# Optimization experiments

Measured on AMD Instinct MI355X. Metric: run time of the kernel, lower is better.

Reference implementation:

```python
import jax, jax.numpy as jnp
import numpy as np

NUM_USERS = 1_000_000
NUM_ITEMS = 500_000
NUM_GENRES = 20
NUM_TAGS = 100
EMBEDDING_DIM = 64
HIDDEN_UNITS = [256, 128, 64]
NUM_CLASSES = 5
BATCH = 16384


def setup_inputs() -> dict:
    key = jax.random.key(0)
    ks = jax.random.split(key, 16)
    deep_in = EMBEDDING_DIM * 2 + NUM_GENRES + NUM_TAGS  # 248
    inp = {
        "user": jax.random.randint(ks[0], (BATCH,), 0, NUM_USERS),
        "item": jax.random.randint(ks[1], (BATCH,), 0, NUM_ITEMS),
        "genre": jax.random.uniform(ks[2], (BATCH, NUM_GENRES), dtype=jnp.float32),
        "tag": jax.random.uniform(ks[3], (BATCH, NUM_TAGS), dtype=jnp.float32),
        # wide Linear(num_users+num_items -> HIDDEN_UNITS[-1]); stored transposed
        # as (vocab, out) so the one-hot matmul becomes a row gather.
        "wide_W": jax.random.normal(ks[4], (NUM_USERS + NUM_ITEMS, HIDDEN_UNITS[-1]), dtype=jnp.float32) * 0.01,
        "wide_b": jnp.zeros((HIDDEN_UNITS[-1],), dtype=jnp.float32),
        "user_emb": jax.random.normal(ks[5], (NUM_USERS, EMBEDDING_DIM), dtype=jnp.float32) * 0.01,
        "item_emb": jax.random.normal(ks[6], (NUM_ITEMS, EMBEDDING_DIM), dtype=jnp.float32) * 0.01,
        "W0": jax.random.normal(ks[7], (deep_in, HIDDEN_UNITS[0]), dtype=jnp.float32) * 0.02,
        "b0": jnp.zeros((HIDDEN_UNITS[0],), dtype=jnp.float32),
        "W1": jax.random.normal(ks[8], (HIDDEN_UNITS[0], HIDDEN_UNITS[1]), dtype=jnp.float32) * 0.02,
        "b1": jnp.zeros((HIDDEN_UNITS[1],), dtype=jnp.float32),
        "W2": jax.random.normal(ks[9], (HIDDEN_UNITS[1], HIDDEN_UNITS[2]), dtype=jnp.float32) * 0.02,
        "b2": jnp.zeros((HIDDEN_UNITS[2],), dtype=jnp.float32),
        "final_W": jax.random.normal(ks[10], (HIDDEN_UNITS[-1] * 2, NUM_CLASSES), dtype=jnp.float32) * 0.02,
        "final_b": jnp.zeros((NUM_CLASSES,), dtype=jnp.float32),
    }
    return inp


def reference(user, item, genre, tag, wide_W, wide_b, user_emb, item_emb,
              W0, b0, W1, b1, W2, b2, final_W, final_b):
    # Wide path: one_hot(user)++one_hot(item) @ W + b  ==  gather+sum of rows.
    wide_out = wide_W[user] + wide_W[NUM_USERS + item] + wide_b  # [B, 64]
    # Deep path (dropout is identity in eval mode).
    u = user_emb[user]   # [B, E]
    v = item_emb[item]   # [B, E]
    h = jnp.concatenate([u, v, genre, tag], axis=1)  # [B, 248]
    h = jax.nn.relu(h @ W0 + b0)
    h = jax.nn.relu(h @ W1 + b1)
    h = jax.nn.relu(h @ W2 + b2)  # [B, 64]
    combined = jnp.concatenate([h, wide_out], axis=1)  # [B, 128]
    logits = combined @ final_W + final_b  # [B, NUM_CLASSES]
    return logits
```

## Files before the change

### kernel.cpp

```cpp
#include <hip/hip_runtime.h>

#define BATCH 16384
#define NU 1000000
#define TBR 32
#define MT 512
#define WSOFF0 0
#define WSOFF1 65536
#define WSOFF2 98304
#define WSREQ  212992

typedef __attribute__((ext_vector_type(8))) short short8;
typedef __attribute__((ext_vector_type(4))) short short4v;
typedef __attribute__((ext_vector_type(4))) float f32x4;

__device__ __forceinline__ unsigned short f32_bf16(float f) {
    unsigned int u = __float_as_uint(f);
    u += 0x7FFF + ((u >> 16) & 1);
    return (unsigned short)(u >> 16);
}
__device__ __forceinline__ float bf16_f32(unsigned short h) {
    return __uint_as_float(((unsigned int)h) << 16);
}

__device__ __forceinline__ int swz(int row, int byteInRow, int rowStrideB) {
    return row * rowStrideB + (byteInRow ^ ((row & 7) << 4));
}

__device__ __forceinline__ short8 cvt8(float4 a, float4 b) {
    short8 s;
    s[0] = (short)f32_bf16(a.x); s[1] = (short)f32_bf16(a.y);
    s[2] = (short)f32_bf16(a.z); s[3] = (short)f32_bf16(a.w);
    s[4] = (short)f32_bf16(b.x); s[5] = (short)f32_bf16(b.y);
    s[6] = (short)f32_bf16(b.z); s[7] = (short)f32_bf16(b.w);
    return s;
}

__global__ void prep_weights(const float* __restrict__ W0, const float* __restrict__ W1,
                             const float* __restrict__ W2, unsigned short* __restrict__ ws)
{
    __shared__ float t[64 * 65];
    int b = blockIdx.x;
    const float* src; unsigned short* dst; int K, N, K2, k0, n0;
    if (b < 16)      { src = W0; dst = ws + WSOFF0; K = 248; N = 256; K2 = 256; k0 = (b >> 2) * 64; n0 = (b & 3) * 64; }
    else if (b < 24) { int i = b - 16; src = W1; dst = ws + WSOFF1; K = 256; N = 128; K2 = 256; k0 = (i >> 1) * 64; n0 = (i & 1) * 64; }
    else             { int i = b - 24; src = W2; dst = ws + WSOFF2; K = 128; N = 64;  K2 = 128; k0 = i * 64; n0 = 0; }

    int tid = threadIdx.x;
    for (int q = tid; q < 64 * 16; q += 256) {
        int k = q >> 4, nq = q & 15;
        float4 v = make_float4(0.f, 0.f, 0.f, 0.f);
        if (k0 + k < K) v = *(const float4*)(src + (size_t)(k0 + k) * N + n0 + nq * 4);
        t[k * 65 + nq * 4 + 0] = v.x;
        t[k * 65 + nq * 4 + 1] = v.y;
        t[k * 65 + nq * 4 + 2] = v.z;
        t[k * 65 + nq * 4 + 3] = v.w;
    }
    __syncthreads();
    for (int q = tid; q < 64 * 8; q += 256) {
        int n = q >> 3, kg = q & 7;
        short8 o;
        #pragma unroll
        for (int i = 0; i < 8; ++i) o[i] = (short)f32_bf16(t[(kg * 8 + i) * 65 + n]);
        *(short8*)(dst + (size_t)(n0 + n) * K2 + k0 + kg * 8) = o;
    }
}

__global__ __launch_bounds__(MT) void wd_mfma(
        const int* __restrict__ user, const int* __restrict__ item,
        const float* __restrict__ genre, const float* __restrict__ tag,
        const float* __restrict__ wide_W, const float* __restrict__ wide_b,
        const float* __restrict__ user_emb, const float* __restrict__ item_emb,
        const float* __restrict__ b0, const float* __restrict__ b1,
        const float* __restrict__ b2,
        const float* __restrict__ fW, const float* __restrict__ fb,
        const unsigned short* __restrict__ ws, float* __restrict__ out)
{
    __shared__ unsigned short sX[TBR * 256];
    __shared__ unsigned short sH0[TBR * 256];
    __shared__ unsigned short sH1[TBR * 128];
    __shared__ unsigned short sH2[TBR * 72];
    __shared__ unsigned short sWide[TBR * 72];

    const int tid = threadIdx.x;
    const int row0 = blockIdx.x * TBR;
    const unsigned short* w0t = ws + WSOFF0;
    const unsigned short* w1t = ws + WSOFF1;
    const unsigned short* w2t = ws + WSOFF2;

    for (int q = tid; q < TBR * 32; q += MT) {
        int r = q >> 5, j = q & 31;
        int grow = row0 + r;
        float4 va = make_float4(0.f, 0.f, 0.f, 0.f);
        float4 vb = va;
        if (j < 8) {
            const float4* p = (const float4*)(user_emb + (size_t)user[grow] * 64);
            va = p[j * 2]; vb = p[j * 2 + 1];
        } else if (j < 16) {
            const float4* p = (const float4*)(item_emb + (size_t)item[grow] * 64);
            va = p[(j - 8) * 2]; vb = p[(j - 8) * 2 + 1];
        } else if (j == 16) {
            const float4* p = (const float4*)(genre + (size_t)grow * 20);
            va = p[0]; vb = p[1];
        } else if (j == 17) {
            const float4* p = (const float4*)(genre + (size_t)grow * 20);
            va = p[2]; vb = p[3];
        } else if (j == 18) {
            va = *(const float4*)(genre + (size_t)grow * 20 + 16);
            vb = *(const float4*)(tag + (size_t)grow * 100);
        } else if (j < 31) {
            const float4* p = (const float4*)(tag + (size_t)grow * 100 + 4);
            int jj = j - 19;
            va = p[jj * 2]; vb = p[jj * 2 + 1];
        }
        *(short8*)((char*)sX + swz(r, j * 16, 512)) = cvt8(va, vb);
    }

    for (int q = tid; q < TBR * 16; q += MT) {
        int r = q >> 4, j = q & 15;
        int grow = row0 + r;
        float4 a = ((const float4*)(wide_W + (size_t)user[grow] * 64))[j];
        float4 b = ((const float4*)(wide_W + (size_t)(NU + item[grow]) * 64))[j];
        float4 c = ((const float4*)wide_b)[j];
        short4v o;
        o[0] = (short)f32_bf16(a.x + b.x + c.x);
        o[1] = (short)f32_bf16(a.y + b.y + c.y);
        o[2] = (short)f32_bf16(a.z + b.z + c.z);
        o[3] = (short)f32_bf16(a.w + b.w + c.w);
        *(short4v*)(sWide + r * 72 + j * 4) = o;
    }
    __syncthreads();

    const int wid = tid >> 6;
    const int lane = tid & 63;
    const int lr = lane & 15;
    const int lh = lane >> 4;

    {
        const int cbase = wid * 32;
        f32x4 acc[2][2];
        #pragma unroll
        for (int rt = 0; rt < 2; ++rt)
            #pragma unroll
            for (int t = 0; t < 2; ++t) acc[rt][t] = (f32x4)(0.f);

        #pragma unroll
        for (int kc = 0; kc < 8; ++kc) {
            const int kb = kc * 32 + lh * 8;
            short8 a[2];
            #pragma unroll
            for (int rt = 0; rt < 2; ++rt)
                a[rt] = *(const short8*)((const char*)sX + swz(rt * 16 + lr, kb * 2, 512));
            #pragma unroll
            for (int t = 0; t < 2; ++t) {
                short8 bf = *(const short8*)(w0t + (size_t)(cbase + t * 16 + lr) * 256 + kb);
                #pragma unroll
                for (int rt = 0; rt < 2; ++rt)
                    acc[rt][t] = __builtin_amdgcn_mfma_f32_16x16x32_bf16(a[rt], bf, acc[rt][t], 0, 0, 0);
            }
        }
        #pragma unroll
        for (int t = 0; t < 2; ++t) {
            float bias = b0[cbase + t * 16 + lr];
            #pragma unroll
            for (int rt = 0; rt < 2; ++rt)
                #pragma unroll
                for (int jj = 0; jj < 4; ++jj) {
                    int row = rt * 16 + lh * 4 + jj;
                    float v = fmaxf(acc[rt][t][jj] + bias, 0.f);
                    *(unsigned short*)((char*)sH0 + swz(row, (cbase + t * 16 + lr) * 2, 512)) = f32_bf16(v);
                }
        }
        __syncthreads();
    }

    {
        const int cbase = wid * 16;
        f32x4 acc[2];
        acc[0] = (f32x4)(0.f); acc[1] = (f32x4)(0.f);

        #pragma unroll
        for (int kc = 0; kc < 8; ++kc) {
            const int kb = kc * 32 + lh * 8;
            short8 a[2];
            #pragma unroll
            for (int rt = 0; rt < 2; ++rt)
                a[rt] = *(const short8*)((const char*)sH0 + swz(rt * 16 + lr, kb * 2, 512));
            short8 bf = *(const short8*)(w1t + (size_t)(cbase + lr) * 256 + kb);
            #pragma unroll
            for (int rt = 0; rt < 2; ++rt)
                acc[rt] = __builtin_amdgcn_mfma_f32_16x16x32_bf16(a[rt], bf, acc[rt], 0, 0, 0);
        }
        float bias = b1[cbase + lr];
        #pragma unroll
        for (int rt = 0; rt < 2; ++rt)
            #pragma unroll
            for (int jj = 0; jj < 4; ++jj) {
                int row = rt * 16 + lh * 4 + jj;
                float v = fmaxf(acc[rt][jj] + bias, 0.f);
                *(unsigned short*)((char*)sH1 + swz(row, (cbase + lr) * 2, 256)) = f32_bf16(v);
            }
        __syncthreads();
    }

    {
        const int t = wid & 3;
        const int rtb = wid >> 2;
        const int cbase = t * 16;
        f32x4 acc = (f32x4)(0.f);

        #pragma unroll
        for (int kc = 0; kc < 4; ++kc) {
            const int kb = kc * 32 + lh * 8;
            short8 a = *(const short8*)((const char*)sH1 + swz(rtb * 16 + lr, kb * 2, 256));
            short8 bf = *(const short8*)(w2t + (size_t)(cbase + lr) * 128 + kb);
            acc = __builtin_amdgcn_mfma_f32_16x16x32_bf16(a, bf, acc, 0, 0, 0);
        }
        float bias = b2[cbase + lr];
        #pragma unroll
        for (int jj = 0; jj < 4; ++jj) {
            int row = rtb * 16 + lh * 4 + jj;
            sH2[row * 72 + cbase + lr] = f32_bf16(fmaxf(acc[jj] + bias, 0.f));
        }
        __syncthreads();
    }

    if (tid < TBR * 5) {
        int r = tid / 5, c = tid - r * 5;
        float acc = fb[c];
        #pragma unroll
        for (int kq = 0; kq < 8; ++kq) {
            short8 h = *(const short8*)(sH2 + r * 72 + kq * 8);
            #pragma unroll
            for (int i = 0; i < 8; ++i)
                acc = fmaf(bf16_f32((unsigned short)h[i]), fW[(kq * 8 + i) * 5 + c], acc);
        }
        #pragma unroll
        for (int kq = 0; kq < 8; ++kq) {
            short8 h = *(const short8*)(sWide + r * 72 + kq * 8);
            #pragma unroll
            for (int i = 0; i < 8; ++i)
                acc = fmaf(bf16_f32((unsigned short)h[i]), fW[(64 + kq * 8 + i) * 5 + c], acc);
        }
        out[(size_t)(row0 + r) * 5 + c] = acc;
    }
}

#define NTHR 256
#define TB 32

__device__ __forceinline__ void fma4(float4& a, float s, const float4& w) {
    a.x = fmaf(s, w.x, a.x); a.y = fmaf(s, w.y, a.y);
    a.z = fmaf(s, w.z, a.z); a.w = fmaf(s, w.w, a.w);
}
__device__ __forceinline__ float4 add4(const float4& a, const float4& b) {
    return make_float4(a.x + b.x, a.y + b.y, a.z + b.z, a.w + b.w);
}
__device__ __forceinline__ float4 relu4(const float4& a) {
    return make_float4(fmaxf(a.x, 0.f), fmaxf(a.y, 0.f), fmaxf(a.z, 0.f), fmaxf(a.w, 0.f));
}

__global__ void wd_fused(const int* __restrict__ user, const int* __restrict__ item,
                         const float* __restrict__ genre, const float* __restrict__ tag,
                         const float* __restrict__ wide_W, const float* __restrict__ wide_b,
                         const float* __restrict__ user_emb, const float* __restrict__ item_emb,
                         const float* __restrict__ W0, const float* __restrict__ b0,
                         const float* __restrict__ W1, const float* __restrict__ b1,
                         const float* __restrict__ W2, const float* __restrict__ b2,
                         const float* __restrict__ fW, const float* __restrict__ fb,
                         float* __restrict__ out)
{
    __shared__ float sA[TB * 248];
    __shared__ float sB[TB * 256];
    __shared__ float sC[TB * 64];

    const int tid = threadIdx.x;
    const int row0 = blockIdx.x * TB;

    for (int q = tid; q < TB * 62; q += NTHR) {
        int r = q / 62, j = q - r * 62, grow = row0 + r;
        float4 v;
        if (j < 16) v = reinterpret_cast<const float4*>(user_emb + (size_t)user[grow] * 64)[j];
        else if (j < 32) v = reinterpret_cast<const float4*>(item_emb + (size_t)item[grow] * 64)[j - 16];
        else if (j < 37) v = reinterpret_cast<const float4*>(genre + (size_t)grow * 20)[j - 32];
        else v = reinterpret_cast<const float4*>(tag + (size_t)grow * 100)[j - 37];
        *reinterpret_cast<float4*>(sA + r * 248 + j * 4) = v;
    }
    for (int q = tid; q < TB * 16; q += NTHR) {
        int r = q >> 4, j = q & 15, grow = row0 + r;
        float4 a = reinterpret_cast<const float4*>(wide_W + (size_t)user[grow] * 64)[j];
        float4 b = reinterpret_cast<const float4*>(wide_W + (size_t)(NU + item[grow]) * 64)[j];
        float4 c = reinterpret_cast<const float4*>(wide_b)[j];
        *reinterpret_cast<float4*>(sC + r * 64 + j * 4) =
            make_float4(a.x + b.x + c.x, a.y + b.y + c.y, a.z + b.z + c.z, a.w + b.w + c.w);
    }
    __syncthreads();
    {
        const int cg = tid & 63, r0 = (tid >> 6) * 8;
        float4 acc[8];
        #pragma unroll
        for (int r = 0; r < 8; ++r) acc[r] = make_float4(0.f, 0.f, 0.f, 0.f);
        for (int k = 0; k < 248; k += 4) {
            const float4* wp = reinterpret_cast<const float4*>(W0 + (size_t)k * 256) + cg;
            float4 w0 = wp[0], w1 = wp[64], w2 = wp[128], w3 = wp[192];
            #pragma unroll
            for (int r = 0; r < 8; ++r) {
                float4 xv = *reinterpret_cast<const float4*>(sA + (r0 + r) * 248 + k);
                fma4(acc[r], xv.x, w0); fma4(acc[r], xv.y, w1);
                fma4(acc[r], xv.z, w2); fma4(acc[r], xv.w, w3);
            }
        }
        float4 bb = reinterpret_cast<const float4*>(b0)[cg];
        #pragma unroll
        for (int r = 0; r < 8; ++r)
            *reinterpret_cast<float4*>(sB + (r0 + r) * 256 + cg * 4) = relu4(add4(acc[r], bb));
    }
    __syncthreads();
    {
        const int cg = tid & 31, r0 = (tid >> 5) * 4;
        float4 acc[4];
        #pragma unroll
        for (int r = 0; r < 4; ++r) acc[r] = make_float4(0.f, 0.f, 0.f, 0.f);
        for (int k = 0; k < 256; k += 4) {
            const float4* wp = reinterpret_cast<const float4*>(W1 + (size_t)k * 128) + cg;
            float4 w0 = wp[0], w1 = wp[32], w2 = wp[64], w3 = wp[96];
            #pragma unroll
            for (int r = 0; r < 4; ++r) {
                float4 xv = *reinterpret_cast<const float4*>(sB + (r0 + r) * 256 + k);
                fma4(acc[r], xv.x, w0); fma4(acc[r], xv.y, w1);
                fma4(acc[r], xv.z, w2); fma4(acc[r], xv.w, w3);
            }
        }
        float4 bb = reinterpret_cast<const float4*>(b1)[cg];
        #pragma unroll
        for (int r = 0; r < 4; ++r)
            *reinterpret_cast<float4*>(sA + (r0 + r) * 128 + cg * 4) = relu4(add4(acc[r], bb));
    }
    __syncthreads();
    {
        const int cg = tid & 15, r0 = (tid >> 4) * 2;
        float4 acc[2];
        acc[0] = make_float4(0.f, 0.f, 0.f, 0.f); acc[1] = acc[0];
        for (int k = 0; k < 128; k += 4) {
            const float4* wp = reinterpret_cast<const float4*>(W2 + (size_t)k * 64) + cg;
            float4 w0 = wp[0], w1 = wp[16], w2 = wp[32], w3 = wp[48];
            #pragma unroll
            for (int r = 0; r < 2; ++r) {
                float4 xv = *reinterpret_cast<const float4*>(sA + (r0 + r) * 128 + k);
                fma4(acc[r], xv.x, w0); fma4(acc[r], xv.y, w1);
                fma4(acc[r], xv.z, w2); fma4(acc[r], xv.w, w3);
            }
        }
        float4 bb = reinterpret_cast<const float4*>(b2)[cg];
        #pragma unroll
        for (int r = 0; r < 2; ++r)
            *reinterpret_cast<float4*>(sB + (r0 + r) * 64 + cg * 4) = relu4(add4(acc[r], bb));
    }
    __syncthreads();
    if (tid < TB * 5) {
        int r = tid / 5, c = tid - r * 5;
        float acc = fb[c];
        for (int k = 0; k < 64; ++k) acc = fmaf(sB[r * 64 + k], fW[k * 5 + c], acc);
        for (int k = 0; k < 64; ++k) acc = fmaf(sC[r * 64 + k], fW[(64 + k) * 5 + c], acc);
        out[(size_t)(row0 + r) * 5 + c] = acc;
    }
}

extern "C" void kernel_launch(void* const* d_in, const int* in_sizes, int n_in,
                              void* d_out, int out_size, void* d_ws, size_t ws_size,
                              hipStream_t stream) {
    const int* user = (const int*)d_in[0];
    const int* item = (const int*)d_in[1];
    const float* genre = (const float*)d_in[2];
    const float* tag = (const float*)d_in[3];
    const float* wide_W = (const float*)d_in[4];
    const float* wide_b = (const float*)d_in[5];
    const float* user_emb = (const float*)d_in[6];
    const float* item_emb = (const float*)d_in[7];
    const float* W0 = (const float*)d_in[8];
    const float* b0 = (const float*)d_in[9];
    const float* W1 = (const float*)d_in[10];
    const float* b1 = (const float*)d_in[11];
    const float* W2 = (const float*)d_in[12];
    const float* b2 = (const float*)d_in[13];
    const float* fW = (const float*)d_in[14];
    const float* fb = (const float*)d_in[15];
    float* out = (float*)d_out;

    if (ws_size >= (size_t)WSREQ) {
        hipLaunchKernelGGL(prep_weights, dim3(26), dim3(256), 0, stream,
                           W0, W1, W2, (unsigned short*)d_ws);
        hipLaunchKernelGGL(wd_mfma, dim3(BATCH / TBR), dim3(MT), 0, stream,
                           user, item, genre, tag, wide_W, wide_b, user_emb, item_emb,
                           b0, b1, b2, fW, fb, (const unsigned short*)d_ws, out);
    } else {
        hipLaunchKernelGGL(wd_fused, dim3(BATCH / TB), dim3(NTHR), 0, stream,
                           user, item, genre, tag, wide_W, wide_b, user_emb, item_emb,
                           W0, b0, W1, b1, W2, b2, fW, fb, out);
    }
}
```

Measured before the change: 34.36 us.

## Double rows per block, preload layer weights into registers, stage final weights in LDS

Rows per block go from 32 to 64. Each wave now loads its W0 and W1 bf16 fragments and the biases into registers once, before the gather phase, so those global weight loads overlap the embedding gathers. Each fragment is then reused across four row tiles instead of two. The gather loops are fully unrolled into a fixed six iterations, and the final 640-float weight matrix is staged in shared memory. The kernel launches half as many blocks, and launch_bounds(512,1) plus the larger register weight arrays raise register use and lower occupancy. That may reduce latency hiding for the random gathers.

```diff
diff --git a/kernel.cpp b/kernel.cpp
--- a/kernel.cpp
+++ b/kernel.cpp
@@ -2,7 +2,7 @@
 
 #define BATCH 16384
 #define NU 1000000
-#define TBR 32
+#define TBR 64
 #define MT 512
 #define WSOFF0 0
 #define WSOFF1 65536
@@ -65,7 +65,7 @@
     }
 }
 
-__global__ __launch_bounds__(MT) void wd_mfma(
+__global__ __launch_bounds__(MT, 1) void wd_mfma(
         const int* __restrict__ user, const int* __restrict__ item,
         const float* __restrict__ genre, const float* __restrict__ tag,
         const float* __restrict__ wide_W, const float* __restrict__ wide_b,
@@ -80,6 +80,7 @@
     __shared__ unsigned short sH1[TBR * 128];
     __shared__ unsigned short sH2[TBR * 72];
     __shared__ unsigned short sWide[TBR * 72];
+    __shared__ float sFW[640];
 
     const int tid = threadIdx.x;
     const int row0 = blockIdx.x * TBR;
@@ -87,140 +88,162 @@
     const unsigned short* w1t = ws + WSOFF1;
     const unsigned short* w2t = ws + WSOFF2;
 
-    for (int q = tid; q < TBR * 32; q += MT) {
-        int r = q >> 5, j = q & 31;
-        int grow = row0 + r;
-        float4 va = make_float4(0.f, 0.f, 0.f, 0.f);
-        float4 vb = va;
-        if (j < 8) {
-            const float4* p = (const float4*)(user_emb + (size_t)user[grow] * 64);
-            va = p[j * 2]; vb = p[j * 2 + 1];
-        } else if (j < 16) {
-            const float4* p = (const float4*)(item_emb + (size_t)item[grow] * 64);
-            va = p[(j - 8) * 2]; vb = p[(j - 8) * 2 + 1];
-        } else if (j == 16) {
-            const float4* p = (const float4*)(genre + (size_t)grow * 20);
-            va = p[0]; vb = p[1];
-        } else if (j == 17) {
-            const float4* p = (const float4*)(genre + (size_t)grow * 20);
-            va = p[2]; vb = p[3];
-        } else if (j == 18) {
-            va = *(const float4*)(genre + (size_t)grow * 20 + 16);
-            vb = *(const float4*)(tag + (size_t)grow * 100);
-        } else if (j < 31) {
-            const float4* p = (const float4*)(tag + (size_t)grow * 100 + 4);
-            int jj = j - 19;
-            va = p[jj * 2]; vb = p[jj * 2 + 1];
-        }
-        *(short8*)((char*)sX + swz(r, j * 16, 512)) = cvt8(va, vb);
-    }
-
-    for (int q = tid; q < TBR * 16; q += MT) {
-        int r = q >> 4, j = q & 15;
-        int grow = row0 + r;
-        float4 a = ((const float4*)(wide_W + (size_t)user[grow] * 64))[j];
-        float4 b = ((const float4*)(wide_W + (size_t)(NU + item[grow]) * 64))[j];
-        float4 c = ((const float4*)wide_b)[j];
-        short4v o;
-        o[0] = (short)f32_bf16(a.x + b.x + c.x);
-        o[1] = (short)f32_bf16(a.y + b.y + c.y);
-        o[2] = (short)f32_bf16(a.z + b.z + c.z);
-        o[3] = (short)f32_bf16(a.w + b.w + c.w);
-        *(short4v*)(sWide + r * 72 + j * 4) = o;
-    }
-    __syncthreads();
-
     const int wid = tid >> 6;
     const int lane = tid & 63;
     const int lr = lane & 15;
     const int lh = lane >> 4;
 
-    {
-        const int cbase = wid * 32;
-        f32x4 acc[2][2];
-        #pragma unroll
-        for (int rt = 0; rt < 2; ++rt)
+    const int cb0 = wid * 32;
+    const int cb1 = wid * 16;
+    short8 B0[2][8];
+    #pragma unroll
+    for (int t = 0; t < 2; ++t)
+        #pragma unroll
+        for (int kc = 0; kc < 8; ++kc)
+            B0[t][kc] = *(const short8*)(w0t + (size_t)(cb0 + t * 16 + lr) * 256 + kc * 32 + lh * 8);
+    short8 B1[8];
+    #pragma unroll
+    for (int kc = 0; kc < 8; ++kc)
+        B1[kc] = *(const short8*)(w1t + (size_t)(cb1 + lr) * 256 + kc * 32 + lh * 8);
+    float rb0[2];
+    rb0[0] = b0[cb0 + lr]; rb0[1] = b0[cb0 + 16 + lr];
+    float rb1 = b1[cb1 + lr];
+    float rb2 = b2[(wid & 3) * 16 + lr];
+
+    #pragma unroll
+    for (int it = 0; it < 6; ++it) {
+        int q = tid + it * MT;
+        if (it < 4) {
+            int r = q >> 5, j = q & 31;
+            int grow = row0 + r;
+            float4 va = make_float4(0.f, 0.f, 0.f, 0.f);
+            float4 vb = va;
+            if (j < 8) {
+                const float4* p = (const float4*)(user_emb + (size_t)user[grow] * 64);
+                va = p[j * 2]; vb = p[j * 2 + 1];
+            } else if (j < 16) {
+                const float4* p = (const float4*)(item_emb + (size_t)item[grow] * 64);
+                va = p[(j - 8) * 2]; vb = p[(j - 8) * 2 + 1];
+            } else if (j == 16) {
+                const float4* p = (const float4*)(genre + (size_t)grow * 20);
+                va = p[0]; vb = p[1];
+            } else if (j == 17) {
+                const float4* p = (const float4*)(genre + (size_t)grow * 20);
+                va = p[2]; vb = p[3];
+            } else if (j == 18) {
+                va = *(const float4*)(genre + (size_t)grow * 20 + 16);
+                vb = *(const float4*)(tag + (size_t)grow * 100);
+            } else if (j < 31) {
+                const float4* p = (const float4*)(tag + (size_t)grow * 100 + 4);
+                int jj = j - 19;
+                va = p[jj * 2]; vb = p[jj * 2 + 1];
+            }
+            *(short8*)((char*)sX + swz(r, j * 16, 512)) = cvt8(va, vb);
+        } else {
+            int p = q - 4 * MT;
+            int r = p >> 4, j = p & 15;
+            int grow = row0 + r;
+            float4 a = ((const float4*)(wide_W + (size_t)user[grow] * 64))[j];
+            float4 b = ((const float4*)(wide_W + (size_t)(NU + item[grow]) * 64))[j];
+            float4 c = ((const float4*)wide_b)[j];
+            short4v o;
+            o[0] = (short)f32_bf16(a.x + b.x + c.x);
+            o[1] = (short)f32_bf16(a.y + b.y + c.y);
+            o[2] = (short)f32_bf16(a.z + b.z + c.z);
+            o[3] = (short)f32_bf16(a.w + b.w + c.w);
+            *(short4v*)(sWide + r * 72 + j * 4) = o;
+        }
+    }
+    if (tid < 160) {
+        ((float4*)sFW)[tid] = ((const float4*)fW)[tid];
+    }
+    __syncthreads();
+
+    {
+        f32x4 acc[4][2];
+        #pragma unroll
+        for (int rt = 0; rt < 4; ++rt)
             #pragma unroll
             for (int t = 0; t < 2; ++t) acc[rt][t] = (f32x4)(0.f);
 
         #pragma unroll
         for (int kc = 0; kc < 8; ++kc) {
             const int kb = kc * 32 + lh * 8;
-            short8 a[2];
-            #pragma unroll
-            for (int rt = 0; rt < 2; ++rt)
+            short8 a[4];
+            #pragma unroll
+            for (int rt = 0; rt < 4; ++rt)
                 a[rt] = *(const short8*)((const char*)sX + swz(rt * 16 + lr, kb * 2, 512));
             #pragma unroll
-            for (int t = 0; t < 2; ++t) {
-                short8 bf = *(const short8*)(w0t + (size_t)(cbase + t * 16 + lr) * 256 + kb);
+            for (int t = 0; t < 2; ++t)
                 #pragma unroll
-                for (int rt = 0; rt < 2; ++rt)
-                    acc[rt][t] = __builtin_amdgcn_mfma_f32_16x16x32_bf16(a[rt], bf, acc[rt][t], 0, 0, 0);
-            }
+                for (int rt = 0; rt < 4; ++rt)
+                    acc[rt][t] = __builtin_amdgcn_mfma_f32_16x16x32_bf16(a[rt], B0[t][kc], acc[rt][t], 0, 0, 0);
         }
         #pragma unroll
         for (int t = 0; t < 2; ++t) {
-            float bias = b0[cbase + t * 16 + lr];
-            #pragma unroll
-            for (int rt = 0; rt < 2; ++rt)
+            #pragma unroll
+            for (int rt = 0; rt < 4; ++rt)
                 #pragma unroll
                 for (int jj = 0; jj < 4; ++jj) {
                     int row = rt * 16 + lh * 4 + jj;
-                    float v = fmaxf(acc[rt][t][jj] + bias, 0.f);
-                    *(unsigned short*)((char*)sH0 + swz(row, (cbase + t * 16 + lr) * 2, 512)) = f32_bf16(v);
+                    float v = fmaxf(acc[rt][t][jj] + rb0[t], 0.f);
+                    *(unsigned short*)((char*)sH0 + swz(row, (cb0 + t * 16 + lr) * 2, 512)) = f32_bf16(v);
                 }
         }
         __syncthreads();
     }
 
     {
-        const int cbase = wid * 16;
+        f32x4 acc[4];
+        #pragma unroll
+        for (int rt = 0; rt < 4; ++rt) acc[rt] = (f32x4)(0.f);
+
+        #pragma unroll
+        for (int kc = 0; kc < 8; ++kc) {
+            const int kb = kc * 32 + lh * 8;
+            short8 a[4];
+            #pragma unroll
+            for (int rt = 0; rt < 4; ++rt)
+                a[rt] = *(const short8*)((const char*)sH0 + swz(rt * 16 + lr, kb * 2, 512));
+            #pragma unroll
+            for (int rt = 0; rt < 4; ++rt)
+                acc[rt] = __builtin_amdgcn_mfma_f32_16x16x32_bf16(a[rt], B1[kc], acc[rt], 0, 0, 0);
+        }
+        #pragma unroll
+        for (int rt = 0; rt < 4; ++rt)
+            #pragma unroll
+            for (int jj = 0; jj < 4; ++jj) {
+                int row = rt * 16 + lh * 4 + jj;
+                float v = fmaxf(acc[rt][jj] + rb1, 0.f);
+                *(unsigned short*)((char*)sH1 + swz(row, (cb1 + lr) * 2, 256)) = f32_bf16(v);
+            }
+        __syncthreads();
+    }
+
+    {
+        const int t = wid & 3;
+        const int rtb = (wid >> 2) * 2;
+        const int cbase = t * 16;
         f32x4 acc[2];
         acc[0] = (f32x4)(0.f); acc[1] = (f32x4)(0.f);
 
         #pragma unroll
-        for (int kc = 0; kc < 8; ++kc) {
-            const int kb = kc * 32 + lh * 8;
-            short8 a[2];
-            #pragma unroll
-            for (int rt = 0; rt < 2; ++rt)
-                a[rt] = *(const short8*)((const char*)sH0 + swz(rt * 16 + lr, kb * 2, 512));
-            short8 bf = *(const short8*)(w1t + (size_t)(cbase + lr) * 256 + kb);
-            #pragma unroll
-            for (int rt = 0; rt < 2; ++rt)
-                acc[rt] = __builtin_amdgcn_mfma_f32_16x16x32_bf16(a[rt], bf, acc[rt], 0, 0, 0);
-        }
-        float bias = b1[cbase + lr];
-        #pragma unroll
-        for (int rt = 0; rt < 2; ++rt)
-            #pragma unroll
-            for (int jj = 0; jj < 4; ++jj) {
-                int row = rt * 16 + lh * 4 + jj;
-                float v = fmaxf(acc[rt][jj] + bias, 0.f);
-                *(unsigned short*)((char*)sH1 + swz(row, (cbase + lr) * 2, 256)) = f32_bf16(v);
-            }
-        __syncthreads();
-    }
-
-    {
-        const int t = wid & 3;
-        const int rtb = wid >> 2;
-        const int cbase = t * 16;
-        f32x4 acc = (f32x4)(0.f);
-
-        #pragma unroll
         for (int kc = 0; kc < 4; ++kc) {
             const int kb = kc * 32 + lh * 8;
-            short8 a = *(const short8*)((const char*)sH1 + swz(rtb * 16 + lr, kb * 2, 256));
             short8 bf = *(const short8*)(w2t + (size_t)(cbase + lr) * 128 + kb);
-            acc = __builtin_amdgcn_mfma_f32_16x16x32_bf16(a, bf, acc, 0, 0, 0);
-        }
-        float bias = b2[cbase + lr];
-        #pragma unroll
-        for (int jj = 0; jj < 4; ++jj) {
-            int row = rtb * 16 + lh * 4 + jj;
-            sH2[row * 72 + cbase + lr] = f32_bf16(fmaxf(acc[jj] + bias, 0.f));
-        }
+            #pragma unroll
+            for (int rr = 0; rr < 2; ++rr) {
+                short8 a = *(const short8*)((const char*)sH1 + swz((rtb + rr) * 16 + lr, kb * 2, 256));
+                acc[rr] = __builtin_amdgcn_mfma_f32_16x16x32_bf16(a, bf, acc[rr], 0, 0, 0);
+            }
+        }
+        #pragma unroll
+        for (int rr = 0; rr < 2; ++rr)
+            #pragma unroll
+            for (int jj = 0; jj < 4; ++jj) {
+                int row = (rtb + rr) * 16 + lh * 4 + jj;
+                sH2[row * 72 + cbase + lr] = f32_bf16(fmaxf(acc[rr][jj] + rb2, 0.f));
+            }
         __syncthreads();
     }
 
@@ -232,14 +255,14 @@
             short8 h = *(const short8*)(sH2 + r * 72 + kq * 8);
             #pragma unroll
             for (int i = 0; i < 8; ++i)
-                acc = fmaf(bf16_f32((unsigned short)h[i]), fW[(kq * 8 + i) * 5 + c], acc);
+                acc = fmaf(bf16_f32((unsigned short)h[i]), sFW[(kq * 8 + i) * 5 + c], acc);
         }
         #pragma unroll
         for (int kq = 0; kq < 8; ++kq) {
             short8 h = *(const short8*)(sWide + r * 72 + kq * 8);
             #pragma unroll
             for (int i = 0; i < 8; ++i)
-                acc = fmaf(bf16_f32((unsigned short)h[i]), fW[(64 + kq * 8 + i) * 5 + c], acc);
+                acc = fmaf(bf16_f32((unsigned short)h[i]), sFW[(64 + kq * 8 + i) * 5 + c], acc);
         }
         out[(size_t)(row0 + r) * 5 + c] = acc;
     }
```

New measurement: 30.87 us. -10.2%, faster.

## Double rows per block, preload layer-0 weights in registers, simplify weight prep

Applied to the files above, without the earlier changes.

Doubles the rows per block to 64 with 1024 threads and reassigns warps so each warp computes one 16-column slice of layer 0 across all four row tiles. That warp's layer-0 B fragments and the biases are loaded into registers up front, so their global loads overlap the embedding gathers. The final-layer weights are staged in shared memory. The weight prep kernel is replaced by a simpler per-thread transpose that needs no shared memory, spread over more blocks. The costs are fewer blocks (256), higher register pressure, and less coalesced reads in the prep kernel.

```diff
diff --git a/kernel.cpp b/kernel.cpp
--- a/kernel.cpp
+++ b/kernel.cpp
@@ -2,8 +2,8 @@
 
 #define BATCH 16384
 #define NU 1000000
-#define TBR 32
-#define MT 512
+#define TBR 64
+#define MT 1024
 #define WSOFF0 0
 #define WSOFF1 65536
 #define WSOFF2 98304
@@ -35,34 +35,26 @@
     return s;
 }
 
-__global__ void prep_weights(const float* __restrict__ W0, const float* __restrict__ W1,
-                             const float* __restrict__ W2, unsigned short* __restrict__ ws)
-{
-    __shared__ float t[64 * 65];
-    int b = blockIdx.x;
-    const float* src; unsigned short* dst; int K, N, K2, k0, n0;
-    if (b < 16)      { src = W0; dst = ws + WSOFF0; K = 248; N = 256; K2 = 256; k0 = (b >> 2) * 64; n0 = (b & 3) * 64; }
-    else if (b < 24) { int i = b - 16; src = W1; dst = ws + WSOFF1; K = 256; N = 128; K2 = 256; k0 = (i >> 1) * 64; n0 = (i & 1) * 64; }
-    else             { int i = b - 24; src = W2; dst = ws + WSOFF2; K = 128; N = 64;  K2 = 128; k0 = i * 64; n0 = 0; }
-
-    int tid = threadIdx.x;
-    for (int q = tid; q < 64 * 16; q += 256) {
-        int k = q >> 4, nq = q & 15;
-        float4 v = make_float4(0.f, 0.f, 0.f, 0.f);
-        if (k0 + k < K) v = *(const float4*)(src + (size_t)(k0 + k) * N + n0 + nq * 4);
-        t[k * 65 + nq * 4 + 0] = v.x;
-        t[k * 65 + nq * 4 + 1] = v.y;
-        t[k * 65 + nq * 4 + 2] = v.z;
-        t[k * 65 + nq * 4 + 3] = v.w;
-    }
-    __syncthreads();
-    for (int q = tid; q < 64 * 8; q += 256) {
-        int n = q >> 3, kg = q & 7;
-        short8 o;
-        #pragma unroll
-        for (int i = 0; i < 8; ++i) o[i] = (short)f32_bf16(t[(kg * 8 + i) * 65 + n]);
-        *(short8*)(dst + (size_t)(n0 + n) * K2 + k0 + kg * 8) = o;
-    }
+__device__ __forceinline__ void prep_slice(int g, const float* __restrict__ W0,
+                                           const float* __restrict__ W1,
+                                           const float* __restrict__ W2,
+                                           unsigned short* __restrict__ ws) {
+    if (g >= 53248) return;
+    int item = g >> 2, pair = g & 3;
+    const float* src; unsigned short* dst; int n, kg, K, N, K2;
+    if (item < 8192)       { src = W0; dst = ws + WSOFF0; n = item >> 5;            kg = item & 31; K = 248; N = 256; K2 = 256; }
+    else if (item < 12288) { int r = item - 8192;  src = W1; dst = ws + WSOFF1; n = r >> 5; kg = r & 31; K = 256; N = 128; K2 = 256; }
+    else                   { int r = item - 12288; src = W2; dst = ws + WSOFF2; n = r >> 4; kg = r & 15; K = 128; N = 64;  K2 = 128; }
+    int k0 = kg * 8 + pair * 2;
+    float v0 = (k0 < K)     ? src[(size_t)k0 * N + n]       : 0.f;
+    float v1 = (k0 + 1 < K) ? src[(size_t)(k0 + 1) * N + n] : 0.f;
+    unsigned int packed = (unsigned int)f32_bf16(v0) | ((unsigned int)f32_bf16(v1) << 16);
+    *(unsigned int*)(dst + (size_t)n * K2 + k0) = packed;
+}
+
+__global__ void prep_simple(const float* __restrict__ W0, const float* __restrict__ W1,
+                            const float* __restrict__ W2, unsigned short* __restrict__ ws) {
+    prep_slice(blockIdx.x * 512 + threadIdx.x, W0, W1, W2, ws);
 }
 
 __global__ __launch_bounds__(MT) void wd_mfma(
@@ -80,6 +72,7 @@
     __shared__ unsigned short sH1[TBR * 128];
     __shared__ unsigned short sH2[TBR * 72];
     __shared__ unsigned short sWide[TBR * 72];
+    __shared__ float sFW[640];
 
     const int tid = threadIdx.x;
     const int row0 = blockIdx.x * TBR;
@@ -87,7 +80,28 @@
     const unsigned short* w1t = ws + WSOFF1;
     const unsigned short* w2t = ws + WSOFF2;
 
-    for (int q = tid; q < TBR * 32; q += MT) {
+    const int wid = tid >> 6;
+    const int lane = tid & 63;
+    const int lr = lane & 15;
+    const int lh = lane >> 4;
+
+    const int cb0 = wid * 16;
+    const int s1 = wid & 7, h1 = wid >> 3;
+    const int cb1 = s1 * 16;
+    const int s2 = wid & 3, q2 = wid >> 2;
+    const int cb2 = s2 * 16;
+
+    short8 B0[8];
+    #pragma unroll
+    for (int kc = 0; kc < 8; ++kc)
+        B0[kc] = *(const short8*)(w0t + (size_t)(cb0 + lr) * 256 + kc * 32 + lh * 8);
+    float rb0 = b0[cb0 + lr];
+    float rb1 = b1[cb1 + lr];
+    float rb2 = b2[cb2 + lr];
+
+    #pragma unroll
+    for (int it = 0; it < 2; ++it) {
+        int q = tid + it * MT;
         int r = q >> 5, j = q & 31;
         int grow = row0 + r;
         float4 va = make_float4(0.f, 0.f, 0.f, 0.f);
@@ -114,9 +128,8 @@
         }
         *(short8*)((char*)sX + swz(r, j * 16, 512)) = cvt8(va, vb);
     }
-
-    for (int q = tid; q < TBR * 16; q += MT) {
-        int r = q >> 4, j = q & 15;
+    {
+        int r = tid >> 4, j = tid & 15;
         int grow = row0 + r;
         float4 a = ((const float4*)(wide_W + (size_t)user[grow] * 64))[j];
         float4 b = ((const float4*)(wide_W + (size_t)(NU + item[grow]) * 64))[j];
@@ -128,98 +141,72 @@
         o[3] = (short)f32_bf16(a.w + b.w + c.w);
         *(short4v*)(sWide + r * 72 + j * 4) = o;
     }
-    __syncthreads();
-
-    const int wid = tid >> 6;
-    const int lane = tid & 63;
-    const int lr = lane & 15;
-    const int lh = lane >> 4;
-
-    {
-        const int cbase = wid * 32;
-        f32x4 acc[2][2];
-        #pragma unroll
-        for (int rt = 0; rt < 2; ++rt)
-            #pragma unroll
-            for (int t = 0; t < 2; ++t) acc[rt][t] = (f32x4)(0.f);
-
+    if (tid < 160) {
+        ((float4*)sFW)[tid] = ((const float4*)fW)[tid];
+    }
+    __syncthreads();
+
+    {
+        f32x4 acc[4];
+        #pragma unroll
+        for (int rt = 0; rt < 4; ++rt) acc[rt] = (f32x4)(0.f);
         #pragma unroll
         for (int kc = 0; kc < 8; ++kc) {
             const int kb = kc * 32 + lh * 8;
-            short8 a[2];
-            #pragma unroll
-            for (int rt = 0; rt < 2; ++rt)
-                a[rt] = *(const short8*)((const char*)sX + swz(rt * 16 + lr, kb * 2, 512));
-            #pragma unroll
-            for (int t = 0; t < 2; ++t) {
-                short8 bf = *(const short8*)(w0t + (size_t)(cbase + t * 16 + lr) * 256 + kb);
-                #pragma unroll
-                for (int rt = 0; rt < 2; ++rt)
-                    acc[rt][t] = __builtin_amdgcn_mfma_f32_16x16x32_bf16(a[rt], bf, acc[rt][t], 0, 0, 0);
-            }
-        }
-        #pragma unroll
-        for (int t = 0; t < 2; ++t) {
-            float bias = b0[cbase + t * 16 + lr];
-            #pragma unroll
-            for (int rt = 0; rt < 2; ++rt)
-                #pragma unroll
-                for (int jj = 0; jj < 4; ++jj) {
-                    int row = rt * 16 + lh * 4 + jj;
-                    float v = fmaxf(acc[rt][t][jj] + bias, 0.f);
-                    *(unsigned short*)((char*)sH0 + swz(row, (cbase + t * 16 + lr) * 2, 512)) = f32_bf16(v);
-                }
-        }
+            #pragma unroll
+            for (int rt = 0; rt < 4; ++rt) {
+                short8 a = *(const short8*)((const char*)sX + swz(rt * 16 + lr, kb * 2, 512));
+                acc[rt] = __builtin_amdgcn_mfma_f32_16x16x32_bf16(a, B0[kc], acc[rt], 0, 0, 0);
+            }
+        }
+        #pragma unroll
+        for (int rt = 0; rt < 4; ++rt)
+            #pragma unroll
+            for (int jj = 0; jj < 4; ++jj) {
+                int row = rt * 16 + lh * 4 + jj;
+                float v = fmaxf(acc[rt][jj] + rb0, 0.f);
+                *(unsigned short*)((char*)sH0 + swz(row, (cb0 + lr) * 2, 512)) = f32_bf16(v);
+            }
         __syncthreads();
     }
 
     {
-        const int cbase = wid * 16;
         f32x4 acc[2];
         acc[0] = (f32x4)(0.f); acc[1] = (f32x4)(0.f);
-
         #pragma unroll
         for (int kc = 0; kc < 8; ++kc) {
             const int kb = kc * 32 + lh * 8;
-            short8 a[2];
-            #pragma unroll
-            for (int rt = 0; rt < 2; ++rt)
-                a[rt] = *(const short8*)((const char*)sH0 + swz(rt * 16 + lr, kb * 2, 512));
-            short8 bf = *(const short8*)(w1t + (size_t)(cbase + lr) * 256 + kb);
-            #pragma unroll
-            for (int rt = 0; rt < 2; ++rt)
-                acc[rt] = __builtin_amdgcn_mfma_f32_16x16x32_bf16(a[rt], bf, acc[rt], 0, 0, 0);
-        }
-        float bias = b1[cbase + lr];
+            short8 bf = *(const short8*)(w1t + (size_t)(cb1 + lr) * 256 + kb);
+            #pragma unroll
+            for (int rt = 0; rt < 2; ++rt) {
+                short8 a = *(const short8*)((const char*)sH0 + swz(h1 * 32 + rt * 16 + lr, kb * 2, 512));
+                acc[rt] = __builtin_amdgcn_mfma_f32_16x16x32_bf16(a, bf, acc[rt], 0, 0, 0);
+            }
+        }
         #pragma unroll
         for (int rt = 0; rt < 2; ++rt)
             #pragma unroll
             for (int jj = 0; jj < 4; ++jj) {
-                int row = rt * 16 + lh * 4 + jj;
-                float v = fmaxf(acc[rt][jj] + bias, 0.f);
-                *(unsigned short*)((char*)sH1 + swz(row, (cbase + lr) * 2, 256)) = f32_bf16(v);
+                int row = h1 * 32 + rt * 16 + lh * 4 + jj;
+                float v = fmaxf(acc[rt][jj] + rb1, 0.f);
+                *(unsigned short*)((char*)sH1 + swz(row, (cb1 + lr) * 2, 256)) = f32_bf16(v);
             }
         __syncthreads();
     }
 
     {
-        const int t = wid & 3;
-        const int rtb = wid >> 2;
-        const int cbase = t * 16;
         f32x4 acc = (f32x4)(0.f);
-
         #pragma unroll
         for (int kc = 0; kc < 4; ++kc) {
             const int kb = kc * 32 + lh * 8;
-            short8 a = *(const short8*)((const char*)sH1 + swz(rtb * 16 + lr, kb * 2, 256));
-            short8 bf = *(const short8*)(w2t + (size_t)(cbase + lr) * 128 + kb);
+            short8 bf = *(const short8*)(w2t + (size_t)(cb2 + lr) * 128 + kb);
+            short8 a = *(const short8*)((const char*)sH1 + swz(q2 * 16 + lr, kb * 2, 256));
             acc = __builtin_amdgcn_mfma_f32_16x16x32_bf16(a, bf, acc, 0, 0, 0);
         }
-        float bias = b2[cbase + lr];
         #pragma unroll
         for (int jj = 0; jj < 4; ++jj) {
-            int row = rtb * 16 + lh * 4 + jj;
-            sH2[row * 72 + cbase + lr] = f32_bf16(fmaxf(acc[jj] + bias, 0.f));
+            int row = q2 * 16 + lh * 4 + jj;
+            sH2[row * 72 + cb2 + lr] = f32_bf16(fmaxf(acc[jj] + rb2, 0.f));
         }
         __syncthreads();
     }
@@ -232,14 +219,14 @@
             short8 h = *(const short8*)(sH2 + r * 72 + kq * 8);
             #pragma unroll
             for (int i = 0; i < 8; ++i)
-                acc = fmaf(bf16_f32((unsigned short)h[i]), fW[(kq * 8 + i) * 5 + c], acc);
+                acc = fmaf(bf16_f32((unsigned short)h[i]), sFW[(kq * 8 + i) * 5 + c], acc);
         }
         #pragma unroll
         for (int kq = 0; kq < 8; ++kq) {
             short8 h = *(const short8*)(sWide + r * 72 + kq * 8);
             #pragma unroll
             for (int i = 0; i < 8; ++i)
-                acc = fmaf(bf16_f32((unsigned short)h[i]), fW[(64 + kq * 8 + i) * 5 + c], acc);
+                acc = fmaf(bf16_f32((unsigned short)h[i]), sFW[(64 + kq * 8 + i) * 5 + c], acc);
         }
         out[(size_t)(row0 + r) * 5 + c] = acc;
     }
@@ -387,11 +374,12 @@
     float* out = (float*)d_out;
 
     if (ws_size >= (size_t)WSREQ) {
-        hipLaunchKernelGGL(prep_weights, dim3(26), dim3(256), 0, stream,
-                           W0, W1, W2, (unsigned short*)d_ws);
+        unsigned short* ws = (unsigned short*)d_ws;
+        hipLaunchKernelGGL(prep_simple, dim3(104), dim3(512), 0, stream,
+                           W0, W1, W2, ws);
         hipLaunchKernelGGL(wd_mfma, dim3(BATCH / TBR), dim3(MT), 0, stream,
                            user, item, genre, tag, wide_W, wide_b, user_emb, item_emb,
-                           b0, b1, b2, fW, fb, (const unsigned short*)d_ws, out);
+                           b0, b1, b2, fW, fb, ws, out);
     } else {
         hipLaunchKernelGGL(wd_fused, dim3(BATCH / TB), dim3(NTHR), 0, stream,
                            user, item, genre, tag, wide_W, wide_b, user_emb, item_emb,
```

Measured after the change: 30.35 us. 11.7% less time.
